# Performance work log

Hardware: AMD Instinct MI355X
Metric: run time of the kernel (lower is better)

Reference implementation:

```python
import jax, jax.numpy as jnp
import numpy as np

B, T, D, H = 4, 1024, 1024, 16
HD = D // H  # 64
EPS = 1e-5


def _layernorm(x, g, b):
    mu = jnp.mean(x, axis=-1, keepdims=True)
    var = jnp.mean(jnp.square(x - mu), axis=-1, keepdims=True)
    return (x - mu) * jax.lax.rsqrt(var + EPS) * g + b


def _apply_rope(x, cos, sin):
    # x: (B, H, T, HD); cos/sin: (T, HD//2)
    d = x.shape[-1] // 2
    x1, x2 = x[..., :d], x[..., d:]
    cos = cos[None, None]
    sin = sin[None, None]
    return jnp.concatenate([x1 * cos - x2 * sin, x1 * sin + x2 * cos], axis=-1)


def setup_inputs() -> dict:
    key = jax.random.key(0)
    ks = jax.random.split(key, 8)
    s = 0.02
    x = jax.random.normal(ks[0], (B, T, D), jnp.float32)
    # RoPE tables
    pos = jnp.arange(T, dtype=jnp.float32)
    inv_freq = 1.0 / (10000.0 ** (jnp.arange(HD // 2, dtype=jnp.float32) / (HD // 2)))
    ang = pos[:, None] * inv_freq[None, :]  # (T, HD//2)
    rope_cos, rope_sin = jnp.cos(ang), jnp.sin(ang)
    # causal mask: True = masked out (module does ~attn_mask before SDPA)
    attn_mask = jnp.triu(jnp.ones((T, T), dtype=bool), k=1)
    params = dict(
        ln1_g=jnp.ones((D,), jnp.float32), ln1_b=jnp.zeros((D,), jnp.float32),
        w_qkv=jax.random.normal(ks[1], (D, 3 * D), jnp.float32) * s,
        b_qkv=jnp.zeros((3 * D,), jnp.float32),
        w_out=jax.random.normal(ks[2], (D, D), jnp.float32) * s,
        b_out=jnp.zeros((D,), jnp.float32),
        ln2_g=jnp.ones((D,), jnp.float32), ln2_b=jnp.zeros((D,), jnp.float32),
        w1=jax.random.normal(ks[3], (D, 4 * D), jnp.float32) * s,
        b1=jnp.zeros((4 * D,), jnp.float32),
        w2=jax.random.normal(ks[4], (4 * D, D), jnp.float32) * s,
        b2=jnp.zeros((D,), jnp.float32),
    )
    return dict(x=x, attn_mask=attn_mask, rope_cos=rope_cos, rope_sin=rope_sin, **params)


def reference(x, attn_mask, rope_cos, rope_sin, ln1_g, ln1_b, w_qkv, b_qkv,
              w_out, b_out, ln2_g, ln2_b, w1, b1, w2, b2):
    b, t, d = x.shape
    h = _layernorm(x, ln1_g, ln1_b)
    qkv = (h @ w_qkv + b_qkv).reshape(b, t, 3, H, HD)
    q, k, v = jnp.transpose(qkv, (2, 0, 3, 1, 4))  # each (B, H, T, HD)
    q = _apply_rope(q, rope_cos, rope_sin)
    k = _apply_rope(k, rope_cos, rope_sin)
    scale = 1.0 / jnp.sqrt(jnp.asarray(HD, x.dtype))
    scores = jnp.einsum('bhqd,bhkd->bhqk', q, k) * scale
    allowed = ~attn_mask  # True = attend
    neg = jnp.finfo(scores.dtype).min
    scores = jnp.where(allowed[None, None], scores, neg)
    probs = jax.nn.softmax(scores, axis=-1)
    attn = jnp.einsum('bhqk,bhkd->bhqd', probs, v)
    attn = jnp.transpose(attn, (0, 2, 1, 3)).reshape(b, t, d)
    x = x + (attn @ w_out + b_out)
    h2 = _layernorm(x, ln2_g, ln2_b)
    mlp = jax.nn.gelu(h2 @ w1 + b1, approximate=False) @ w2 + b2
    return x + mlp
```

## Files before the change

### kernel.cpp

```cpp
#include <hip/hip_runtime.h>
#include <hip/hip_bf16.h>
#include <cstdint>


typedef __bf16 bf16x8_t __attribute__((ext_vector_type(8)));
typedef float  f32x4_t  __attribute__((ext_vector_type(4)));

#define MFMA16(a, b, c) __builtin_amdgcn_mfma_f32_16x16x32_bf16((a), (b), (c), 0, 0, 0)

static constexpr int Bb = 4, T = 1024, D = 1024, NH = 16, HD = 64;
static constexpr int ROWS = Bb * T;
static constexpr int QKVN = 3 * D;

__device__ __forceinline__ float bf2f(__hip_bfloat16 v) { return __bfloat162float(v); }
__device__ __forceinline__ ushort f2bfbits(float v) {
    __hip_bfloat16 h = __float2bfloat16(v);
    return *reinterpret_cast<ushort*>(&h);
}
__device__ __forceinline__ float loadf(const void* p, size_t i, int isb16) {
    return isb16 ? bf2f(((const __hip_bfloat16*)p)[i]) : ((const float*)p)[i];
}
__device__ __forceinline__ int dtype16(const void* gref) {
    return (((const unsigned*)gref)[0] & 0xFFFFu) != 0u;
}
__device__ __forceinline__ void gld_lds16(const __hip_bfloat16* g, __hip_bfloat16* l) {
    __builtin_amdgcn_global_load_lds(
        (const __attribute__((address_space(1))) void*)g,
        (__attribute__((address_space(3))) void*)l, 16, 0, 0);
}

__device__ __forceinline__ void trans_tile(const void* B, __hip_bfloat16* BT,
                                           int K, int N, int k0, int n0, int isb16) {
    __shared__ ushort t[64][68];
#pragma unroll
    for (int it = 0; it < 4; ++it) {
        int gi = threadIdx.x + it * 256;
        int r = gi >> 4, c4 = (gi & 15) * 4;
        if (isb16) {
            ushort4 v = *reinterpret_cast<const ushort4*>(
                (const __hip_bfloat16*)B + (size_t)(k0 + r) * N + n0 + c4);
            t[c4 + 0][r] = v.x; t[c4 + 1][r] = v.y;
            t[c4 + 2][r] = v.z; t[c4 + 3][r] = v.w;
        } else {
            float4 v = *reinterpret_cast<const float4*>(
                (const float*)B + (size_t)(k0 + r) * N + n0 + c4);
            t[c4 + 0][r] = f2bfbits(v.x); t[c4 + 1][r] = f2bfbits(v.y);
            t[c4 + 2][r] = f2bfbits(v.z); t[c4 + 3][r] = f2bfbits(v.w);
        }
    }
    __syncthreads();
#pragma unroll
    for (int it = 0; it < 4; ++it) {
        int gi = threadIdx.x + it * 256;
        int r = gi >> 4, c4 = (gi & 15) * 4;
        ushort4 v;
        v.x = t[r][c4]; v.y = t[r][c4 + 1]; v.z = t[r][c4 + 2]; v.w = t[r][c4 + 3];
        *reinterpret_cast<ushort4*>(
            reinterpret_cast<ushort*>(BT) + (size_t)(n0 + r) * K + k0 + c4) = v;
    }
}

__device__ __forceinline__ void ln_row(const void* x, const void* g, const void* bt,
                                       __hip_bfloat16* out, int row, int isb16) {
    const int tid = threadIdx.x;
    const int lane = tid & 63, w = tid >> 6;

    float v[4];
    if (isb16) {
        ushort4 raw = reinterpret_cast<const ushort4*>((const __hip_bfloat16*)x + (size_t)row * D)[tid];
        v[0] = __uint_as_float(((unsigned)raw.x) << 16);
        v[1] = __uint_as_float(((unsigned)raw.y) << 16);
        v[2] = __uint_as_float(((unsigned)raw.z) << 16);
        v[3] = __uint_as_float(((unsigned)raw.w) << 16);
    } else {
        float4 f = reinterpret_cast<const float4*>((const float*)x + (size_t)row * D)[tid];
        v[0] = f.x; v[1] = f.y; v[2] = f.z; v[3] = f.w;
    }

    float s1 = v[0] + v[1] + v[2] + v[3];
    float s2 = v[0] * v[0] + v[1] * v[1] + v[2] * v[2] + v[3] * v[3];
#pragma unroll
    for (int off = 32; off >= 1; off >>= 1) {
        s1 += __shfl_xor(s1, off, 64);
        s2 += __shfl_xor(s2, off, 64);
    }
    __shared__ float r1[4], r2[4];
    if (lane == 0) { r1[w] = s1; r2[w] = s2; }
    __syncthreads();
    float t1 = r1[0] + r1[1] + r1[2] + r1[3];
    float t2 = r2[0] + r2[1] + r2[2] + r2[3];
    float mu  = t1 * (1.0f / D);
    float var = t2 * (1.0f / D) - mu * mu;
    float rstd = rsqrtf(var + 1e-5f);

    const int c = tid * 4;
#pragma unroll
    for (int j = 0; j < 4; j++) {
        float gv = loadf(g, c + j, isb16), bv = loadf(bt, c + j, isb16);
        out[(size_t)row * D + c + j] = __float2bfloat16((v[j] - mu) * rstd * gv + bv);
    }
}

__global__ __launch_bounds__(256) void transpose_k(const void* __restrict__ B,
                                                   __hip_bfloat16* __restrict__ BT,
                                                   const void* __restrict__ gref,
                                                   int K, int N) {
    trans_tile(B, BT, K, N, blockIdx.y * 64, blockIdx.x * 64, dtype16(gref));
}

__global__ __launch_bounds__(256) void fusedpre_k(const void* w_qkv, const void* w_out,
                                                  const void* w1, const void* w2,
                                                  __hip_bfloat16* wqkvT, __hip_bfloat16* woutT,
                                                  __hip_bfloat16* w1T, __hip_bfloat16* w2T,
                                                  const void* __restrict__ x,
                                                  const void* __restrict__ ln_g,
                                                  const void* __restrict__ ln_b,
                                                  __hip_bfloat16* __restrict__ ln_out,
                                                  const void* __restrict__ gref) {
    const int isb16 = dtype16(gref);
    int bid = blockIdx.x;
    if (bid < 3072) {
        const void* src; __hip_bfloat16* dst; int K, N, l;
        if (bid < 768)       { src = w_qkv; dst = wqkvT; K = 1024; N = 3072; l = bid; }
        else if (bid < 1024) { src = w_out; dst = woutT; K = 1024; N = 1024; l = bid - 768; }
        else if (bid < 2048) { src = w1;    dst = w1T;   K = 1024; N = 4096; l = bid - 1024; }
        else                 { src = w2;    dst = w2T;   K = 4096; N = 1024; l = bid - 2048; }
        const int nb = N / 64;
        trans_tile(src, dst, K, N, (l / nb) * 64, (l % nb) * 64, isb16);
    } else {
        ln_row(x, ln_g, ln_b, ln_out, bid - 3072, isb16);
    }
}

__global__ __launch_bounds__(256) void ln_k(const void* __restrict__ x,
                                            const void* __restrict__ g,
                                            const void* __restrict__ bt,
                                            __hip_bfloat16* __restrict__ out,
                                            const void* __restrict__ gref) {
    ln_row(x, g, bt, out, blockIdx.x, dtype16(gref));
}

template <int MODE, bool SPLIT>
__global__ __launch_bounds__(512, 2) void gemm256_k(const __hip_bfloat16* __restrict__ A,
                                                    const __hip_bfloat16* __restrict__ BT,
                                                    const void* __restrict__ bias,
                                                    void* __restrict__ C,
                                                    const void* __restrict__ gref,
                                                    int M, int N, int Kstride, int klen) {
    extern __shared__ __hip_bfloat16 LDSb[];

    const int tid  = threadIdx.x;
    const int lane = tid & 63, w = tid >> 6;
    const int quad = lane >> 4, l15 = lane & 15;
    const int n0 = blockIdx.x * 256, m0 = blockIdx.y * 256;
    const int wmL = (w >> 2) * 128;
    const int wnL = (w & 3) * 64;
    const int kbase = SPLIT ? blockIdx.z * klen : 0;
    const int NT = klen >> 5;

    const int L0 = w * 1024 + lane * 16;
    const int L1 = L0 + 8192;
    const int r0 = L0 >> 6,  k0e = ((L0 & 63) ^ (((L0 >> 9) & 1) << 5)) >> 1;
    const int r1 = L1 >> 6,  k1e = ((L1 & 63) ^ (((L1 >> 9) & 1) << 5)) >> 1;
    const __hip_bfloat16* AgS0 = A  + (size_t)(m0 + r0) * Kstride + kbase + k0e;
    const __hip_bfloat16* AgS1 = A  + (size_t)(m0 + r1) * Kstride + kbase + k1e;
    const __hip_bfloat16* BgS0 = BT + (size_t)(n0 + r0) * Kstride + kbase + k0e;
    const __hip_bfloat16* BgS1 = BT + (size_t)(n0 + r1) * Kstride + kbase + k1e;
    const int ldst0 = w * 512, ldst1 = w * 512 + 4096;

    const int kofs = (quad * 8) ^ ((l15 & 8) << 1);

    f32x4_t acc[8][4] = {};

#pragma unroll
    for (int t = 0; t < 3; ++t) {
        __hip_bfloat16* sA = LDSb + t * 8192;
        __hip_bfloat16* sB = LDSb + 32768 + t * 8192;
        const int ko = t * 32;
        gld_lds16(AgS0 + ko, sA + ldst0);
        gld_lds16(AgS1 + ko, sA + ldst1);
        gld_lds16(BgS0 + ko, sB + ldst0);
        gld_lds16(BgS1 + ko, sB + ldst1);
    }
    asm volatile("s_waitcnt vmcnt(8)" ::: "memory");
    __builtin_amdgcn_s_barrier();
    __builtin_amdgcn_sched_barrier(0);

    for (int t = 0; t < NT; ++t) {
        if (t) {
            if (t + 2 < NT)      { asm volatile("s_waitcnt vmcnt(8)" ::: "memory"); }
            else if (t + 1 < NT) { asm volatile("s_waitcnt vmcnt(4)" ::: "memory"); }
            else                 { asm volatile("s_waitcnt vmcnt(0)" ::: "memory"); }
            __builtin_amdgcn_s_barrier();
            __builtin_amdgcn_sched_barrier(0);
        }
        if (t + 3 < NT) {
            const int sl = (t + 3) & 3;
            __hip_bfloat16* sA = LDSb + sl * 8192;
            __hip_bfloat16* sB = LDSb + 32768 + sl * 8192;
            const int ko = (t + 3) * 32;
            gld_lds16(AgS0 + ko, sA + ldst0);
            gld_lds16(AgS1 + ko, sA + ldst1);
            gld_lds16(BgS0 + ko, sB + ldst0);
            gld_lds16(BgS1 + ko, sB + ldst1);
        }

        const __hip_bfloat16* sA = LDSb + (t & 3) * 8192;
        const __hip_bfloat16* sB = LDSb + 32768 + (t & 3) * 8192;
        bf16x8_t a[8], b[4];
#pragma unroll
        for (int mf = 0; mf < 8; ++mf)
            a[mf] = *reinterpret_cast<const bf16x8_t*>(&sA[(wmL + mf * 16 + l15) * 32 + kofs]);
#pragma unroll
        for (int nf = 0; nf < 4; ++nf)
            b[nf] = *reinterpret_cast<const bf16x8_t*>(&sB[(wnL + nf * 16 + l15) * 32 + kofs]);
        __builtin_amdgcn_s_setprio(1);
#pragma unroll
        for (int mf = 0; mf < 8; ++mf)
#pragma unroll
            for (int nf = 0; nf < 4; ++nf)
                acc[mf][nf] = MFMA16(a[mf], b[nf], acc[mf][nf]);
        __builtin_amdgcn_s_setprio(0);
    }

    __syncthreads();

    __hip_bfloat16* Cb;
    if constexpr (SPLIT) {
        const int z = blockIdx.z;
        if (z == 0)      Cb = (__hip_bfloat16*)C;
        else if (z == 1) Cb = (__hip_bfloat16*)C + (size_t)M * N;
        else if (z == 2) Cb = (__hip_bfloat16*)const_cast<void*>(bias);
        else             Cb = (__hip_bfloat16*)const_cast<void*>(gref);
    } else {
        Cb = (__hip_bfloat16*)C;
    }
    const int isb16 = (MODE == 3) ? 0 : dtype16(gref);
    __hip_bfloat16* E = LDSb;
#pragma unroll
    for (int nf = 0; nf < 4; ++nf) {
        const int cc = wnL + nf * 16 + l15;
        const float bsv = (MODE == 3) ? 0.0f : loadf(bias, n0 + cc, isb16);
#pragma unroll
        for (int mf = 0; mf < 8; ++mf) {
            const int rbase = wmL + mf * 16 + quad * 4;
#pragma unroll
            for (int r = 0; r < 4; ++r) {
                const int rr = rbase + r;
                float v = acc[mf][nf][r] + bsv;
                if constexpr (MODE == 2)
                    v = 0.5f * v * (1.0f + erff(v * 0.70710678118654752f));
                E[rr * 256 + ((cc + (((rr >> 2) & 15) << 4)) & 255)] = __float2bfloat16(v);
            }
        }
    }
    __syncthreads();
#pragma unroll
    for (int it = 0; it < 16; ++it) {
        const int r = it * 16 + (tid >> 5), c = (tid & 31) * 8;
        const int cs = (c + (((r >> 2) & 15) << 4)) & 255;
        uint4 d = *reinterpret_cast<const uint4*>(&E[r * 256 + cs]);
        *reinterpret_cast<uint4*>(&Cb[(size_t)(m0 + r) * N + n0 + c]) = d;
    }
}

template <int MODE, bool SPLIT>
__global__ __launch_bounds__(256) void gemm_k(const __hip_bfloat16* __restrict__ A,
                                              const __hip_bfloat16* __restrict__ BT,
                                              const void* __restrict__ bias,
                                              void* __restrict__ C,
                                              const void* __restrict__ gref,
                                              int M, int N, int Kstride, int klen,
                                              const void* __restrict__ rc,
                                              const void* __restrict__ rs,
                                              __hip_bfloat16* __restrict__ vT) {
    __shared__ __hip_bfloat16 LB[16384];

    const int tid  = threadIdx.x;
    const int lane = tid & 63, w = tid >> 6;
    const int quad = lane >> 4, l15 = lane & 15;
    const int n0 = blockIdx.x * 128, m0 = blockIdx.y * 128;
    const int wm = (w >> 1) * 64, wn = (w & 1) * 64;
    const int kbase = SPLIT ? blockIdx.z * klen : 0;

    const int srow = lane >> 2, skk = (lane & 3) * 8;
    const __hip_bfloat16* Ag = A  + (size_t)(m0 + w * 16 + srow) * Kstride + kbase + skk;
    const __hip_bfloat16* Bg = BT + (size_t)(n0 + w * 16 + srow) * Kstride + kbase + skk;
    const int lwb = (w * 16) * 32;

    f32x4_t acc[4][4] = {};

    gld_lds16(Ag,                LB + lwb);
    gld_lds16(Ag + 64 * Kstride, LB + lwb + 64 * 32);
    gld_lds16(Bg,                LB + 8192 + lwb);
    gld_lds16(Bg + 64 * Kstride, LB + 8192 + lwb + 64 * 32);
    __syncthreads();

    int p = 0;
    for (int k0 = 0; k0 < klen; k0 += 32) {
        if (k0 + 32 < klen) {
            __hip_bfloat16* An = LB + (p ^ 1) * 4096;
            __hip_bfloat16* Bn = LB + 8192 + (p ^ 1) * 4096;
            gld_lds16(Ag + k0 + 32,                An + lwb);
            gld_lds16(Ag + k0 + 32 + 64 * Kstride, An + lwb + 64 * 32);
            gld_lds16(Bg + k0 + 32,                Bn + lwb);
            gld_lds16(Bg + k0 + 32 + 64 * Kstride, Bn + lwb + 64 * 32);
        }

        const __hip_bfloat16* Ac = LB + p * 4096;
        const __hip_bfloat16* Bc = LB + 8192 + p * 4096;
        bf16x8_t af[4], bfr[4];
#pragma unroll
        for (int t = 0; t < 4; t++) {
            af[t]  = *reinterpret_cast<const bf16x8_t*>(&Ac[(wm + t * 16 + l15) * 32 + quad * 8]);
            bfr[t] = *reinterpret_cast<const bf16x8_t*>(&Bc[(wn + t * 16 + l15) * 32 + quad * 8]);
        }
#pragma unroll
        for (int i = 0; i < 4; i++)
#pragma unroll
            for (int j = 0; j < 4; j++)
                acc[i][j] = MFMA16(af[i], bfr[j], acc[i][j]);

        __syncthreads();
        p ^= 1;
    }

    __hip_bfloat16* Cb;
    if constexpr (SPLIT) {
        const int z = blockIdx.z;
        if (z == 0)      Cb = (__hip_bfloat16*)C;
        else if (z == 1) Cb = (__hip_bfloat16*)C + (size_t)M * N;
        else if (z == 2) Cb = (__hip_bfloat16*)const_cast<void*>(bias);
        else             Cb = (__hip_bfloat16*)const_cast<void*>(gref);
    } else {
        Cb = (__hip_bfloat16*)C;
    }
    const int isb16 = (MODE == 3) ? 0 : dtype16(gref);
    __hip_bfloat16* E = LB;

    if constexpr (MODE == 1) {
        const int sec = n0 >> 10;
#pragma unroll
        for (int j = 0; j < 2; j++) {
            const int cc0 = wn + j * 16 + l15;
            const int cc2 = cc0 + 32;
            const float bs0 = loadf(bias, n0 + cc0, isb16);
            const float bs2 = loadf(bias, n0 + cc2, isb16);
            const int d = j * 16 + l15;
#pragma unroll
            for (int i = 0; i < 4; i++) {
                const int rbase = wm + i * 16 + quad * 4;
#pragma unroll
                for (int r = 0; r < 4; r++) {
                    const int rr = rbase + r;
                    float v0 = acc[i][j][r] + bs0;
                    float v2 = acc[i][j + 2][r] + bs2;
                    if (sec < 2) {
                        const int t = (m0 + rr) & (T - 1);
                        const float cv = loadf(rc, (size_t)t * 32 + d, isb16);
                        const float sv = loadf(rs, (size_t)t * 32 + d, isb16);
                        float o0 = v0 * cv - v2 * sv;
                        float o2 = v0 * sv + v2 * cv;
                        if (sec == 0) { o0 *= 0.125f; o2 *= 0.125f; }
                        v0 = o0; v2 = o2;
                    }
                    E[rr * 128 + ((cc0 + (((rr >> 2) & 7) << 4)) & 127)] = __float2bfloat16(v0);
                    E[rr * 128 + ((cc2 + (((rr >> 2) & 7) << 4)) & 127)] = __float2bfloat16(v2);
                }
            }
        }
    } else {
#pragma unroll
        for (int j = 0; j < 4; j++) {
            const int cc = wn + j * 16 + l15;
            const float bsv = (MODE == 3) ? 0.0f : loadf(bias, n0 + cc, isb16);
#pragma unroll
            for (int i = 0; i < 4; i++) {
                const int rbase = wm + i * 16 + quad * 4;
#pragma unroll
                for (int r = 0; r < 4; r++) {
                    const int rr = rbase + r;
                    float v = acc[i][j][r] + bsv;
                    if constexpr (MODE == 2)
                        v = 0.5f * v * (1.0f + erff(v * 0.70710678118654752f));
                    E[rr * 128 + ((cc + (((rr >> 2) & 7) << 4)) & 127)] = __float2bfloat16(v);
                }
            }
        }
    }
    __syncthreads();
#pragma unroll
    for (int it = 0; it < 8; it++) {
        const int r = it * 16 + (tid >> 4), c = (tid & 15) * 8;
        const int cs = (c + (((r >> 2) & 7) << 4)) & 127;
        uint4 d = *reinterpret_cast<const uint4*>(&E[r * 128 + cs]);
        *reinterpret_cast<uint4*>(&Cb[(size_t)(m0 + r) * N + n0 + c]) = d;
    }

    if constexpr (MODE == 1) {
        if (n0 >= 2 * D) {
            const int bq  = m0 >> 10;
            const int t0  = m0 & (T - 1);
            const int n0v = n0 - 2 * D;
#pragma unroll
            for (int it = 0; it < 8; ++it) {
                const int idx = tid + it * 256;
                const int f   = idx >> 4;
                const int tg  = (idx & 15) * 8;
                alignas(16) ushort pk[8];
#pragma unroll
                for (int kk = 0; kk < 8; ++kk) {
                    const int tt = tg + kk;
                    pk[kk] = reinterpret_cast<const ushort*>(E)[
                        tt * 128 + ((f + (((tt >> 2) & 7) << 4)) & 127)];
                }
                *reinterpret_cast<uint4*>(
                    &vT[((size_t)(bq * 1024 + n0v + f)) * T + t0 + tg]) =
                    *reinterpret_cast<const uint4*>(pk);
            }
        }
    }
}

__global__ __launch_bounds__(256) void reduce4_k(const __hip_bfloat16* __restrict__ p0,
                                                 const __hip_bfloat16* __restrict__ p1,
                                                 const __hip_bfloat16* __restrict__ p2,
                                                 const __hip_bfloat16* __restrict__ p3,
                                                 const void* __restrict__ bias,
                                                 const void* __restrict__ res,
                                                 void* __restrict__ out,
                                                 const void* __restrict__ gref) {
    const int isb16 = dtype16(gref);
    const size_t i = ((size_t)blockIdx.x * 256 + threadIdx.x) * 4;
    ushort4 a = *reinterpret_cast<const ushort4*>(p0 + i);
    ushort4 b = *reinterpret_cast<const ushort4*>(p1 + i);
    ushort4 c = *reinterpret_cast<const ushort4*>(p2 + i);
    ushort4 d = *reinterpret_cast<const ushort4*>(p3 + i);
    const int col = (int)(i & (D - 1));
    float v[4];
    v[0] = __uint_as_float((unsigned)a.x << 16) + __uint_as_float((unsigned)b.x << 16)
         + __uint_as_float((unsigned)c.x << 16) + __uint_as_float((unsigned)d.x << 16);
    v[1] = __uint_as_float((unsigned)a.y << 16) + __uint_as_float((unsigned)b.y << 16)
         + __uint_as_float((unsigned)c.y << 16) + __uint_as_float((unsigned)d.y << 16);
    v[2] = __uint_as_float((unsigned)a.z << 16) + __uint_as_float((unsigned)b.z << 16)
         + __uint_as_float((unsigned)c.z << 16) + __uint_as_float((unsigned)d.z << 16);
    v[3] = __uint_as_float((unsigned)a.w << 16) + __uint_as_float((unsigned)b.w << 16)
         + __uint_as_float((unsigned)c.w << 16) + __uint_as_float((unsigned)d.w << 16);
#pragma unroll
    for (int j = 0; j < 4; j++)
        v[j] += loadf(bias, col + j, isb16) + loadf(res, i + j, isb16);
    if (isb16) {
        ushort4 o;
        o.x = f2bfbits(v[0]); o.y = f2bfbits(v[1]); o.z = f2bfbits(v[2]); o.w = f2bfbits(v[3]);
        *reinterpret_cast<ushort4*>((__hip_bfloat16*)out + i) = o;
    } else {
        float4 o = {v[0], v[1], v[2], v[3]};
        *reinterpret_cast<float4*>((float*)out + i) = o;
    }
}

__global__ __launch_bounds__(256) void gemm64_k(const __hip_bfloat16* __restrict__ A,
                                                const __hip_bfloat16* __restrict__ BT,
                                                const void* __restrict__ bias,
                                                const void* __restrict__ res,
                                                void* __restrict__ C,
                                                const void* __restrict__ gref,
                                                int M, int N, int K, int crow0) {
    __shared__ __hip_bfloat16 LB64[12288];

    const int tid  = threadIdx.x;
    const int lane = tid & 63, w = tid >> 6;
    const int quad = lane >> 4, l15 = lane & 15;
    const int n0 = blockIdx.x * 64, m0 = blockIdx.y * 128;
    const int wm = (w >> 1) * 64, wn = (w & 1) * 32;

    const int srow = lane >> 2, skk = (lane & 3) * 8;
    const __hip_bfloat16* Ag = A  + (size_t)(m0 + w * 16 + srow) * K + skk;
    const __hip_bfloat16* Bg = BT + (size_t)(n0 + w * 16 + srow) * K + skk;
    const int lwb = (w * 16) * 32;

    f32x4_t acc[4][2] = {};

    gld_lds16(Ag,          LB64 + lwb);
    gld_lds16(Ag + 64 * K, LB64 + lwb + 64 * 32);
    gld_lds16(Bg,          LB64 + 8192 + lwb);
    __syncthreads();

    int p = 0;
    for (int k0 = 0; k0 < K; k0 += 32) {
        if (k0 + 32 < K) {
            __hip_bfloat16* An = LB64 + (p ^ 1) * 4096;
            __hip_bfloat16* Bn = LB64 + 8192 + (p ^ 1) * 2048;
            gld_lds16(Ag + k0 + 32,          An + lwb);
            gld_lds16(Ag + k0 + 32 + 64 * K, An + lwb + 64 * 32);
            gld_lds16(Bg + k0 + 32,          Bn + lwb);
        }

        const __hip_bfloat16* Ac = LB64 + p * 4096;
        const __hip_bfloat16* Bc = LB64 + 8192 + p * 2048;
        bf16x8_t af[4], bfr[2];
#pragma unroll
        for (int t = 0; t < 4; t++)
            af[t]  = *reinterpret_cast<const bf16x8_t*>(&Ac[(wm + t * 16 + l15) * 32 + quad * 8]);
#pragma unroll
        for (int t = 0; t < 2; t++)
            bfr[t] = *reinterpret_cast<const bf16x8_t*>(&Bc[(wn + t * 16 + l15) * 32 + quad * 8]);
#pragma unroll
        for (int i = 0; i < 4; i++)
#pragma unroll
            for (int j = 0; j < 2; j++)
                acc[i][j] = MFMA16(af[i], bfr[j], acc[i][j]);

        __syncthreads();
        p ^= 1;
    }

    const int isb16 = dtype16(gref);
    __hip_bfloat16* E = LB64;
#pragma unroll
    for (int j = 0; j < 2; j++) {
        const int cc = wn + j * 16 + l15;
        const float bsv = loadf(bias, n0 + cc, isb16);
#pragma unroll
        for (int i = 0; i < 4; i++) {
            const int rbase = wm + i * 16 + quad * 4;
#pragma unroll
            for (int r = 0; r < 4; r++) {
                const int rr = rbase + r;
                E[rr * 64 + ((cc + (((rr >> 2) & 7) << 4)) & 63)] =
                    __float2bfloat16(acc[i][j][r] + bsv);
            }
        }
    }
    __syncthreads();
#pragma unroll
    for (int it = 0; it < 4; it++) {
        const int r = it * 32 + (tid >> 3), c = (tid & 7) * 8;
        const int cs = (c + (((r >> 2) & 7) << 4)) & 63;
        const size_t gr = (size_t)(crow0 + m0 + r);
        alignas(16) ushort pk[8];
        *reinterpret_cast<uint4*>(pk) = *reinterpret_cast<const uint4*>(&E[r * 64 + cs]);
        if (isb16) {
            const ushort4 rv0 = *reinterpret_cast<const ushort4*>(
                (const __hip_bfloat16*)res + gr * N + n0 + c);
            const ushort4 rv1 = *reinterpret_cast<const ushort4*>(
                (const __hip_bfloat16*)res + gr * N + n0 + c + 4);
            const ushort rvs[8] = {rv0.x, rv0.y, rv0.z, rv0.w, rv1.x, rv1.y, rv1.z, rv1.w};
            alignas(16) ushort o[8];
#pragma unroll
            for (int k = 0; k < 8; k++)
                o[k] = f2bfbits(__uint_as_float((unsigned)pk[k] << 16) +
                                __uint_as_float((unsigned)rvs[k] << 16));
            *reinterpret_cast<uint4*>((__hip_bfloat16*)C + gr * N + n0 + c) =
                *reinterpret_cast<const uint4*>(o);
        } else {
            const float4 r0 = *reinterpret_cast<const float4*>(
                (const float*)res + gr * N + n0 + c);
            const float4 r1 = *reinterpret_cast<const float4*>(
                (const float*)res + gr * N + n0 + c + 4);
            const float rf[8] = {r0.x, r0.y, r0.z, r0.w, r1.x, r1.y, r1.z, r1.w};
            float ov[8];
#pragma unroll
            for (int k = 0; k < 8; k++)
                ov[k] = __uint_as_float((unsigned)pk[k] << 16) + rf[k];
            float4 s0 = {ov[0], ov[1], ov[2], ov[3]};
            float4 s1 = {ov[4], ov[5], ov[6], ov[7]};
            *reinterpret_cast<float4*>((float*)C + gr * N + n0 + c)     = s0;
            *reinterpret_cast<float4*>((float*)C + gr * N + n0 + c + 4) = s1;
        }
    }
}

__global__ __launch_bounds__(256) void ropevt_k(__hip_bfloat16* __restrict__ qkv,
                                                const void* __restrict__ rc,
                                                const void* __restrict__ rs,
                                                __hip_bfloat16* __restrict__ vT,
                                                const void* __restrict__ gref) {
    const int bid = blockIdx.x;
    if (bid < 8192) {
        const int isb16 = dtype16(gref);
        const int id = bid * 256 + threadIdx.x;
        const int d  = id & 31;
        const int h  = (id >> 5) & 15;
        const int t  = (id >> 9) & 1023;
        const int b  = id >> 19;
        const float c = loadf(rc, t * 32 + d, isb16);
        const float s = loadf(rs, t * 32 + d, isb16);
        __hip_bfloat16* base = qkv + ((size_t)(b * T + t)) * QKVN + h * HD + d;
        float x1 = bf2f(base[0]), x2 = bf2f(base[32]);
        base[0]  = __float2bfloat16((x1 * c - x2 * s) * 0.125f);
        base[32] = __float2bfloat16((x1 * s + x2 * c) * 0.125f);
        float y1 = bf2f(base[D]), y2 = bf2f(base[D + 32]);
        base[D]      = __float2bfloat16(y1 * c - y2 * s);
        base[D + 32] = __float2bfloat16(y1 * s + y2 * c);
    } else {
        __shared__ ushort t[64][65];
        const int l = bid - 8192;
        const int t0 = (l & 15) * 64, bh = l >> 4;
        const int b = bh >> 4, h = bh & 15;
        const __hip_bfloat16* src = qkv + ((size_t)b * T) * QKVN + 2 * D + h * HD;
#pragma unroll
        for (int it = 0; it < 16; ++it) {
            int idx = threadIdx.x + it * 256;
            int r = idx >> 6, d = idx & 63;
            t[d][r] = *reinterpret_cast<const ushort*>(src + (size_t)(t0 + r) * QKVN + d);
        }
        __syncthreads();
#pragma unroll
        for (int it = 0; it < 16; ++it) {
            int idx = threadIdx.x + it * 256;
            int r = idx >> 6, c = idx & 63;
            reinterpret_cast<ushort*>(vT)[((size_t)bh * 64 + r) * T + t0 + c] = t[r][c];
        }
    }
}

__global__ __launch_bounds__(256) void flash_k(const __hip_bfloat16* __restrict__ qkv,
                                               const __hip_bfloat16* __restrict__ vT,
                                               __hip_bfloat16* __restrict__ out) {
    __shared__ __hip_bfloat16 Qs[2][64 * 32];
    __shared__ __hip_bfloat16 Ks[2][2][64 * 32];
    __shared__ __hip_bfloat16 Vs[2][2][64 * 32];
    __shared__ __hip_bfloat16 Ps[4][2][16 * 32];

    const int tid = threadIdx.x;
    const int bid = blockIdx.x;
    const int qt = 15 - (bid >> 6);
    const int bh = bid & 63;
    const int b = bh >> 4, h = bh & 15;
    const int q0 = qt * 64;
    const int lane = tid & 63, w = tid >> 6, quad = lane >> 4, l15 = lane & 15;
    const int srow = lane >> 2, skk = (lane & 3) * 8;

    const __hip_bfloat16* qg = qkv + ((size_t)(b * T) + q0 + w * 16 + srow) * QKVN + h * HD + skk;
    const __hip_bfloat16* kg = qkv + ((size_t)(b * T) + w * 16 + srow) * QKVN + D + h * HD + skk;
    const __hip_bfloat16* vg = vT + ((size_t)bh * 64 + w * 16 + srow) * T + skk;

    gld_lds16(qg,      &Qs[0][(w * 16) * 32]);
    gld_lds16(qg + 32, &Qs[1][(w * 16) * 32]);
    gld_lds16(kg,      &Ks[0][0][(w * 16) * 32]);
    gld_lds16(kg + 32, &Ks[0][1][(w * 16) * 32]);
    gld_lds16(vg,      &Vs[0][0][(w * 16) * 32]);
    gld_lds16(vg + 32, &Vs[0][1][(w * 16) * 32]);
    __syncthreads();

    const bf16x8_t aq0 = *reinterpret_cast<const bf16x8_t*>(&Qs[0][(w * 16 + l15) * 32 + quad * 8]);
    const bf16x8_t aq1 = *reinterpret_cast<const bf16x8_t*>(&Qs[1][(w * 16 + l15) * 32 + quad * 8]);

    float m_run[4], l_run[4];
    f32x4_t o[4] = {};
#pragma unroll
    for (int i = 0; i < 4; i++) { m_run[i] = -1e30f; l_run[i] = 0.0f; }

    int p = 0;
    for (int kt = 0; kt <= qt; kt++) {
        if (kt < qt) {
            const size_t ko = (size_t)(kt + 1) * 64;
            gld_lds16(kg + ko * QKVN,      &Ks[p ^ 1][0][(w * 16) * 32]);
            gld_lds16(kg + ko * QKVN + 32, &Ks[p ^ 1][1][(w * 16) * 32]);
            gld_lds16(vg + ko,             &Vs[p ^ 1][0][(w * 16) * 32]);
            gld_lds16(vg + ko + 32,        &Vs[p ^ 1][1][(w * 16) * 32]);
        }

        f32x4_t s[4];
#pragma unroll
        for (int c = 0; c < 4; c++) {
            f32x4_t z = {};
            bf16x8_t k0f = *reinterpret_cast<const bf16x8_t*>(&Ks[p][0][(c * 16 + l15) * 32 + quad * 8]);
            bf16x8_t k1f = *reinterpret_cast<const bf16x8_t*>(&Ks[p][1][(c * 16 + l15) * 32 + quad * 8]);
            z = MFMA16(aq0, k0f, z);
            z = MFMA16(aq1, k1f, z);
            s[c] = z;
        }

        if (kt == qt) {
#pragma unroll
            for (int c = 0; c < 4; c++)
#pragma unroll
                for (int i = 0; i < 4; i++) {
                    int rr = w * 16 + quad * 4 + i;
                    int cc = c * 16 + l15;
                    if (cc > rr) s[c][i] = -1e30f;
                }
        }

        float mnew[4], alpha[4];
#pragma unroll
        for (int i = 0; i < 4; i++) {
            float mx = fmaxf(fmaxf(s[0][i], s[1][i]), fmaxf(s[2][i], s[3][i]));
#pragma unroll
            for (int off = 1; off < 16; off <<= 1) mx = fmaxf(mx, __shfl_xor(mx, off, 64));
            mnew[i] = fmaxf(m_run[i], mx);
            alpha[i] = __expf(m_run[i] - mnew[i]);
            m_run[i] = mnew[i];
        }
#pragma unroll
        for (int c = 0; c < 4; c++)
#pragma unroll
            for (int i = 0; i < 4; i++) s[c][i] = __expf(s[c][i] - mnew[i]);
#pragma unroll
        for (int i = 0; i < 4; i++) {
            float sm = s[0][i] + s[1][i] + s[2][i] + s[3][i];
#pragma unroll
            for (int off = 1; off < 16; off <<= 1) sm += __shfl_xor(sm, off, 64);
            l_run[i] = l_run[i] * alpha[i] + sm;
#pragma unroll
            for (int od = 0; od < 4; od++) o[od][i] *= alpha[i];
        }

#pragma unroll
        for (int c = 0; c < 4; c++)
#pragma unroll
            for (int i = 0; i < 4; i++)
                Ps[w][c >> 1][(quad * 4 + i) * 32 + (c & 1) * 16 + l15] =
                    __float2bfloat16(s[c][i]);

        bf16x8_t ap0 = *reinterpret_cast<const bf16x8_t*>(&Ps[w][0][l15 * 32 + quad * 8]);
        bf16x8_t ap1 = *reinterpret_cast<const bf16x8_t*>(&Ps[w][1][l15 * 32 + quad * 8]);
#pragma unroll
        for (int od = 0; od < 4; od++) {
            bf16x8_t v0f = *reinterpret_cast<const bf16x8_t*>(&Vs[p][0][(od * 16 + l15) * 32 + quad * 8]);
            bf16x8_t v1f = *reinterpret_cast<const bf16x8_t*>(&Vs[p][1][(od * 16 + l15) * 32 + quad * 8]);
            o[od] = MFMA16(ap0, v0f, o[od]);
            o[od] = MFMA16(ap1, v1f, o[od]);
        }

        __syncthreads();
        p ^= 1;
    }

#pragma unroll
    for (int od = 0; od < 4; od++)
#pragma unroll
        for (int i = 0; i < 4; i++) {
            int row = q0 + w * 16 + quad * 4 + i;
            int col = h * HD + od * 16 + l15;
            float v = o[od][i] / l_run[i];
            out[((size_t)b * T + row) * D + col] = __float2bfloat16(v);
        }
}

extern "C" void kernel_launch(void* const* d_in, const int* in_sizes, int n_in,
                              void* d_out, int out_size, void* d_ws, size_t ws_size,
                              hipStream_t stream) {
    const int o = (in_sizes[1] == T * (HD / 2)) ? 1 : 2;
    const void* x     = d_in[0];
    const void* rc    = d_in[o + 0];
    const void* rs    = d_in[o + 1];
    const void* ln1g  = d_in[o + 2];
    const void* ln1b  = d_in[o + 3];
    const void* w_qkv = d_in[o + 4];
    const void* b_qkv = d_in[o + 5];
    const void* w_out = d_in[o + 6];
    const void* b_out = d_in[o + 7];
    const void* ln2g  = d_in[o + 8];
    const void* ln2b  = d_in[o + 9];
    const void* w1    = d_in[o + 10];
    const void* b1    = d_in[o + 11];
    const void* w2    = d_in[o + 12];
    const void* b2    = d_in[o + 13];

    char* ws = (char*)d_ws;
    const size_t MB = 1024 * 1024;

    static bool attr_done = false;
    if (!attr_done) {
        hipFuncSetAttribute(reinterpret_cast<const void*>(&gemm256_k<2, false>),
                            hipFuncAttributeMaxDynamicSharedMemorySize, 131072);
        hipFuncSetAttribute(reinterpret_cast<const void*>(&gemm256_k<3, true>),
                            hipFuncAttributeMaxDynamicSharedMemorySize, 131072);
        attr_done = true;
    }

    if (ws_size >= 72 * MB + 256) {
        __hip_bfloat16* bufA  = (__hip_bfloat16*)(ws + 256);
        __hip_bfloat16* qkvb  = (__hip_bfloat16*)(ws + 8 * MB + 256);
        __hip_bfloat16* vTb   = (__hip_bfloat16*)(ws + 32 * MB + 256);
        __hip_bfloat16* mid   = qkvb;
        __hip_bfloat16* wqkvT = (__hip_bfloat16*)(ws + 40 * MB + 256);
        __hip_bfloat16* woutT = (__hip_bfloat16*)(ws + 46 * MB + 256);
        __hip_bfloat16* w1T   = (__hip_bfloat16*)(ws + 48 * MB + 256);
        __hip_bfloat16* w2T   = (__hip_bfloat16*)(ws + 56 * MB + 256);
        __hip_bfloat16* part0 = (__hip_bfloat16*)(ws + 40 * MB + 256);
        __hip_bfloat16* part2 = (__hip_bfloat16*)(ws + 64 * MB + 256);
        __hip_bfloat16* part1 = (__hip_bfloat16*)(ws + 48 * MB + 256);
        __hip_bfloat16* part3 = bufA;

        fusedpre_k<<<3072 + ROWS, 256, 0, stream>>>(w_qkv, w_out, w1, w2,
                                                    wqkvT, woutT, w1T, w2T,
                                                    x, ln1g, ln1b, bufA, ln1g);
        gemm_k<1, false><<<dim3(QKVN / 128, ROWS / 128), 256, 0, stream>>>(
            bufA, wqkvT, b_qkv, qkvb, ln1g, ROWS, QKVN, D, D, rc, rs, vTb);
        flash_k<<<16 * Bb * NH, 256, 0, stream>>>(qkvb, vTb, bufA);
        gemm64_k<<<dim3(D / 64, ROWS / 128), 256, 0, stream>>>(bufA, woutT, b_out, x,
                                                               d_out, ln1g, ROWS, D, D, 0);
        ln_k<<<ROWS, 256, 0, stream>>>(d_out, ln2g, ln2b, bufA, ln1g);
        gemm256_k<2, false><<<dim3(4 * D / 256, ROWS / 256), 512, 131072, stream>>>(
            bufA, w1T, b1, mid, ln1g, ROWS, 4 * D, D, D);
        gemm256_k<3, true><<<dim3(D / 256, ROWS / 256, 4), 512, 131072, stream>>>(
            mid, w2T, part2, part0, part3, ROWS, D, 4 * D, D);
        reduce4_k<<<(ROWS * D) / (256 * 4), 256, 0, stream>>>(part0, part1, part2, part3,
                                                              b2, d_out, d_out, ln1g);
    } else {
        __hip_bfloat16* bufA  = (__hip_bfloat16*)(ws + 256);
        __hip_bfloat16* qkvb  = (__hip_bfloat16*)(ws + 8 * MB + 256);
        __hip_bfloat16* wqkvT = (__hip_bfloat16*)(ws + 32 * MB + 256);
        __hip_bfloat16* vTb   = (__hip_bfloat16*)(ws + 32 * MB + 256);
        __hip_bfloat16* woutT = (__hip_bfloat16*)(ws + 8 * MB + 256);
        __hip_bfloat16* w1T   = (__hip_bfloat16*)(ws + 8 * MB + 256);
        __hip_bfloat16* w2T   = (__hip_bfloat16*)(ws + 16 * MB + 256);
        __hip_bfloat16* mid   = (__hip_bfloat16*)(ws + 24 * MB + 256);

        transpose_k<<<dim3(QKVN / 64, D / 64), 256, 0, stream>>>(w_qkv, wqkvT, ln1g, D, QKVN);
        ln_k<<<ROWS, 256, 0, stream>>>(x, ln1g, ln1b, bufA, ln1g);
        gemm_k<0, false><<<dim3(QKVN / 128, ROWS / 128), 256, 0, stream>>>(
            bufA, wqkvT, b_qkv, qkvb, ln1g, ROWS, QKVN, D, D, nullptr, nullptr, nullptr);
        ropevt_k<<<8192 + 1024, 256, 0, stream>>>(qkvb, rc, rs, vTb, ln1g);
        flash_k<<<16 * Bb * NH, 256, 0, stream>>>(qkvb, vTb, bufA);
        transpose_k<<<dim3(D / 64, D / 64), 256, 0, stream>>>(w_out, woutT, ln1g, D, D);
        gemm64_k<<<dim3(D / 64, ROWS / 128), 256, 0, stream>>>(bufA, woutT, b_out, x,
                                                               d_out, ln1g, ROWS, D, D, 0);
        ln_k<<<ROWS, 256, 0, stream>>>(d_out, ln2g, ln2b, bufA, ln1g);
        transpose_k<<<dim3(4 * D / 64, D / 64), 256, 0, stream>>>(w1, w1T, ln1g, D, 4 * D);
        transpose_k<<<dim3(D / 64, 4 * D / 64), 256, 0, stream>>>(w2, w2T, ln1g, 4 * D, D);
        for (int c = 0; c < 2; c++) {
            const int ro = c * 2048;
            gemm_k<2, false><<<dim3(4 * D / 128, 2048 / 128), 256, 0, stream>>>(
                bufA + (size_t)ro * D, w1T, b1, mid, ln1g, 2048, 4 * D, D, D,
                nullptr, nullptr, nullptr);
            gemm64_k<<<dim3(D / 64, 2048 / 128), 256, 0, stream>>>(mid, w2T, b2, d_out,
                                                                   d_out, ln1g, 2048, D, 4 * D, ro);
        }
    }
}
```

Before: 359.3 us.

## Move weight transposes into flash-attention tail blocks and vectorize LN/reduce stores

Removes the out-proj and MLP weight transposes from the pre-pass kernel and runs them as extra blocks appended to the flash attention launch, sharing one LDS buffer. The aim is to overlap transpose bandwidth work with the imbalanced causal attention tail and to shorten the serial pre-kernel ahead of the QKV GEMM. Layernorm output and the split-K reduce bias/residual loads are also vectorized. Flash LDS usage is unified into one array, and the transpose blocks may compete with attention blocks for CUs.

Measured after the change: 354.2 us. No clear change (-1.4%).

```diff
diff --git a/kernel.cpp b/kernel.cpp
--- a/kernel.cpp
+++ b/kernel.cpp
@@ -29,9 +29,9 @@
         (__attribute__((address_space(3))) void*)l, 16, 0, 0);
 }
 
-__device__ __forceinline__ void trans_tile(const void* B, __hip_bfloat16* BT,
-                                           int K, int N, int k0, int n0, int isb16) {
-    __shared__ ushort t[64][68];
+__device__ __forceinline__ void trans_tile_core(ushort* sc, const void* B,
+                                                __hip_bfloat16* BT,
+                                                int K, int N, int k0, int n0, int isb16) {
 #pragma unroll
     for (int it = 0; it < 4; ++it) {
         int gi = threadIdx.x + it * 256;
@@ -39,13 +39,13 @@
         if (isb16) {
             ushort4 v = *reinterpret_cast<const ushort4*>(
                 (const __hip_bfloat16*)B + (size_t)(k0 + r) * N + n0 + c4);
-            t[c4 + 0][r] = v.x; t[c4 + 1][r] = v.y;
-            t[c4 + 2][r] = v.z; t[c4 + 3][r] = v.w;
+            sc[(c4 + 0) * 68 + r] = v.x; sc[(c4 + 1) * 68 + r] = v.y;
+            sc[(c4 + 2) * 68 + r] = v.z; sc[(c4 + 3) * 68 + r] = v.w;
         } else {
             float4 v = *reinterpret_cast<const float4*>(
                 (const float*)B + (size_t)(k0 + r) * N + n0 + c4);
-            t[c4 + 0][r] = f2bfbits(v.x); t[c4 + 1][r] = f2bfbits(v.y);
-            t[c4 + 2][r] = f2bfbits(v.z); t[c4 + 3][r] = f2bfbits(v.w);
+            sc[(c4 + 0) * 68 + r] = f2bfbits(v.x); sc[(c4 + 1) * 68 + r] = f2bfbits(v.y);
+            sc[(c4 + 2) * 68 + r] = f2bfbits(v.z); sc[(c4 + 3) * 68 + r] = f2bfbits(v.w);
         }
     }
     __syncthreads();
@@ -53,11 +53,16 @@
     for (int it = 0; it < 4; ++it) {
         int gi = threadIdx.x + it * 256;
         int r = gi >> 4, c4 = (gi & 15) * 4;
-        ushort4 v;
-        v.x = t[r][c4]; v.y = t[r][c4 + 1]; v.z = t[r][c4 + 2]; v.w = t[r][c4 + 3];
+        ushort4 v = *reinterpret_cast<const ushort4*>(&sc[r * 68 + c4]);
         *reinterpret_cast<ushort4*>(
             reinterpret_cast<ushort*>(BT) + (size_t)(n0 + r) * K + k0 + c4) = v;
     }
+}
+
+__device__ __forceinline__ void trans_tile(const void* B, __hip_bfloat16* BT,
+                                           int K, int N, int k0, int n0, int isb16) {
+    __shared__ ushort t[64 * 68];
+    trans_tile_core(t, B, BT, K, N, k0, n0, isb16);
 }
 
 __device__ __forceinline__ void ln_row(const void* x, const void* g, const void* bt,
@@ -94,11 +99,19 @@
     float rstd = rsqrtf(var + 1e-5f);
 
     const int c = tid * 4;
-#pragma unroll
-    for (int j = 0; j < 4; j++) {
-        float gv = loadf(g, c + j, isb16), bv = loadf(bt, c + j, isb16);
-        out[(size_t)row * D + c + j] = __float2bfloat16((v[j] - mu) * rstd * gv + bv);
-    }
+    ushort4 o;
+    {
+        float gv, bv;
+        gv = loadf(g, c + 0, isb16); bv = loadf(bt, c + 0, isb16);
+        o.x = f2bfbits((v[0] - mu) * rstd * gv + bv);
+        gv = loadf(g, c + 1, isb16); bv = loadf(bt, c + 1, isb16);
+        o.y = f2bfbits((v[1] - mu) * rstd * gv + bv);
+        gv = loadf(g, c + 2, isb16); bv = loadf(bt, c + 2, isb16);
+        o.z = f2bfbits((v[2] - mu) * rstd * gv + bv);
+        gv = loadf(g, c + 3, isb16); bv = loadf(bt, c + 3, isb16);
+        o.w = f2bfbits((v[3] - mu) * rstd * gv + bv);
+    }
+    *reinterpret_cast<ushort4*>(out + (size_t)row * D + c) = o;
 }
 
 __global__ __launch_bounds__(256) void transpose_k(const void* __restrict__ B,
@@ -108,10 +121,8 @@
     trans_tile(B, BT, K, N, blockIdx.y * 64, blockIdx.x * 64, dtype16(gref));
 }
 
-__global__ __launch_bounds__(256) void fusedpre_k(const void* w_qkv, const void* w_out,
-                                                  const void* w1, const void* w2,
-                                                  __hip_bfloat16* wqkvT, __hip_bfloat16* woutT,
-                                                  __hip_bfloat16* w1T, __hip_bfloat16* w2T,
+__global__ __launch_bounds__(256) void fusedpre_k(const void* w_qkv,
+                                                  __hip_bfloat16* wqkvT,
                                                   const void* __restrict__ x,
                                                   const void* __restrict__ ln_g,
                                                   const void* __restrict__ ln_b,
@@ -119,16 +130,11 @@
                                                   const void* __restrict__ gref) {
     const int isb16 = dtype16(gref);
     int bid = blockIdx.x;
-    if (bid < 3072) {
-        const void* src; __hip_bfloat16* dst; int K, N, l;
-        if (bid < 768)       { src = w_qkv; dst = wqkvT; K = 1024; N = 3072; l = bid; }
-        else if (bid < 1024) { src = w_out; dst = woutT; K = 1024; N = 1024; l = bid - 768; }
-        else if (bid < 2048) { src = w1;    dst = w1T;   K = 1024; N = 4096; l = bid - 1024; }
-        else                 { src = w2;    dst = w2T;   K = 4096; N = 1024; l = bid - 2048; }
-        const int nb = N / 64;
-        trans_tile(src, dst, K, N, (l / nb) * 64, (l % nb) * 64, isb16);
+    if (bid < 768) {
+        const int nb = QKVN / 64;
+        trans_tile(w_qkv, wqkvT, D, QKVN, (bid / nb) * 64, (bid % nb) * 64, isb16);
     } else {
-        ln_row(x, ln_g, ln_b, ln_out, bid - 3072, isb16);
+        ln_row(x, ln_g, ln_b, ln_out, bid - 768, isb16);
     }
 }
 
@@ -446,9 +452,22 @@
          + __uint_as_float((unsigned)c.z << 16) + __uint_as_float((unsigned)d.z << 16);
     v[3] = __uint_as_float((unsigned)a.w << 16) + __uint_as_float((unsigned)b.w << 16)
          + __uint_as_float((unsigned)c.w << 16) + __uint_as_float((unsigned)d.w << 16);
-#pragma unroll
-    for (int j = 0; j < 4; j++)
-        v[j] += loadf(bias, col + j, isb16) + loadf(res, i + j, isb16);
+    float bv[4], rv[4];
+    if (isb16) {
+        ushort4 bb = *reinterpret_cast<const ushort4*>((const __hip_bfloat16*)bias + col);
+        ushort4 rr = *reinterpret_cast<const ushort4*>((const __hip_bfloat16*)res + i);
+        bv[0] = __uint_as_float((unsigned)bb.x << 16); bv[1] = __uint_as_float((unsigned)bb.y << 16);
+        bv[2] = __uint_as_float((unsigned)bb.z << 16); bv[3] = __uint_as_float((unsigned)bb.w << 16);
+        rv[0] = __uint_as_float((unsigned)rr.x << 16); rv[1] = __uint_as_float((unsigned)rr.y << 16);
+        rv[2] = __uint_as_float((unsigned)rr.z << 16); rv[3] = __uint_as_float((unsigned)rr.w << 16);
+    } else {
+        float4 bb = *reinterpret_cast<const float4*>((const float*)bias + col);
+        float4 rr = *reinterpret_cast<const float4*>((const float*)res + i);
+        bv[0] = bb.x; bv[1] = bb.y; bv[2] = bb.z; bv[3] = bb.w;
+        rv[0] = rr.x; rv[1] = rr.y; rv[2] = rr.z; rv[3] = rr.w;
+    }
+#pragma unroll
+    for (int j = 0; j < 4; j++) v[j] += bv[j] + rv[j];
     if (isb16) {
         ushort4 o;
         o.x = f2bfbits(v[0]); o.y = f2bfbits(v[1]); o.z = f2bfbits(v[2]); o.w = f2bfbits(v[3]);
@@ -617,14 +636,35 @@
 
 __global__ __launch_bounds__(256) void flash_k(const __hip_bfloat16* __restrict__ qkv,
                                                const __hip_bfloat16* __restrict__ vT,
-                                               __hip_bfloat16* __restrict__ out) {
-    __shared__ __hip_bfloat16 Qs[2][64 * 32];
-    __shared__ __hip_bfloat16 Ks[2][2][64 * 32];
-    __shared__ __hip_bfloat16 Vs[2][2][64 * 32];
-    __shared__ __hip_bfloat16 Ps[4][2][16 * 32];
-
+                                               __hip_bfloat16* __restrict__ out,
+                                               const void* __restrict__ w_out,
+                                               const void* __restrict__ w1,
+                                               const void* __restrict__ w2,
+                                               __hip_bfloat16* __restrict__ woutT,
+                                               __hip_bfloat16* __restrict__ w1T,
+                                               __hip_bfloat16* __restrict__ w2T,
+                                               const void* __restrict__ gref) {
+    __shared__ __hip_bfloat16 FL[24576];
     const int tid = threadIdx.x;
     const int bid = blockIdx.x;
+
+    if (bid >= 1024) {
+        const int l = bid - 1024;
+        const void* src; __hip_bfloat16* dst; int K, N, ll;
+        if (l < 256)       { src = w_out; dst = woutT; K = 1024; N = 1024; ll = l; }
+        else if (l < 1280) { src = w1;    dst = w1T;   K = 1024; N = 4096; ll = l - 256; }
+        else               { src = w2;    dst = w2T;   K = 4096; N = 1024; ll = l - 1280; }
+        const int nb = N / 64;
+        trans_tile_core(reinterpret_cast<ushort*>(FL), src, dst, K, N,
+                        (ll / nb) * 64, (ll % nb) * 64, dtype16(gref));
+        return;
+    }
+
+    __hip_bfloat16* Qsb = FL;
+    __hip_bfloat16* Ksb = FL + 4096;
+    __hip_bfloat16* Vsb = FL + 12288;
+    __hip_bfloat16* Psb = FL + 20480;
+
     const int qt = 15 - (bid >> 6);
     const int bh = bid & 63;
     const int b = bh >> 4, h = bh & 15;
@@ -636,16 +676,16 @@
     const __hip_bfloat16* kg = qkv + ((size_t)(b * T) + w * 16 + srow) * QKVN + D + h * HD + skk;
     const __hip_bfloat16* vg = vT + ((size_t)bh * 64 + w * 16 + srow) * T + skk;
 
-    gld_lds16(qg,      &Qs[0][(w * 16) * 32]);
-    gld_lds16(qg + 32, &Qs[1][(w * 16) * 32]);
-    gld_lds16(kg,      &Ks[0][0][(w * 16) * 32]);
-    gld_lds16(kg + 32, &Ks[0][1][(w * 16) * 32]);
-    gld_lds16(vg,      &Vs[0][0][(w * 16) * 32]);
-    gld_lds16(vg + 32, &Vs[0][1][(w * 16) * 32]);
+    gld_lds16(qg,      Qsb + (w * 16) * 32);
+    gld_lds16(qg + 32, Qsb + 2048 + (w * 16) * 32);
+    gld_lds16(kg,      Ksb + (w * 16) * 32);
+    gld_lds16(kg + 32, Ksb + 2048 + (w * 16) * 32);
+    gld_lds16(vg,      Vsb + (w * 16) * 32);
+    gld_lds16(vg + 32, Vsb + 2048 + (w * 16) * 32);
     __syncthreads();
 
-    const bf16x8_t aq0 = *reinterpret_cast<const bf16x8_t*>(&Qs[0][(w * 16 + l15) * 32 + quad * 8]);
-    const bf16x8_t aq1 = *reinterpret_cast<const bf16x8_t*>(&Qs[1][(w * 16 + l15) * 32 + quad * 8]);
+    const bf16x8_t aq0 = *reinterpret_cast<const bf16x8_t*>(&Qsb[(w * 16 + l15) * 32 + quad * 8]);
+    const bf16x8_t aq1 = *reinterpret_cast<const bf16x8_t*>(&Qsb[2048 + (w * 16 + l15) * 32 + quad * 8]);
 
     float m_run[4], l_run[4];
     f32x4_t o[4] = {};
@@ -656,18 +696,23 @@
     for (int kt = 0; kt <= qt; kt++) {
         if (kt < qt) {
             const size_t ko = (size_t)(kt + 1) * 64;
-            gld_lds16(kg + ko * QKVN,      &Ks[p ^ 1][0][(w * 16) * 32]);
-            gld_lds16(kg + ko * QKVN + 32, &Ks[p ^ 1][1][(w * 16) * 32]);
-            gld_lds16(vg + ko,             &Vs[p ^ 1][0][(w * 16) * 32]);
-            gld_lds16(vg + ko + 32,        &Vs[p ^ 1][1][(w * 16) * 32]);
-        }
+            __hip_bfloat16* Kn = Ksb + (p ^ 1) * 4096;
+            __hip_bfloat16* Vn = Vsb + (p ^ 1) * 4096;
+            gld_lds16(kg + ko * QKVN,      Kn + (w * 16) * 32);
+            gld_lds16(kg + ko * QKVN + 32, Kn + 2048 + (w * 16) * 32);
+            gld_lds16(vg + ko,             Vn + (w * 16) * 32);
+            gld_lds16(vg + ko + 32,        Vn + 2048 + (w * 16) * 32);
+        }
+
+        const __hip_bfloat16* Kc = Ksb + p * 4096;
+        const __hip_bfloat16* Vc = Vsb + p * 4096;
 
         f32x4_t s[4];
 #pragma unroll
         for (int c = 0; c < 4; c++) {
             f32x4_t z = {};
-            bf16x8_t k0f = *reinterpret_cast<const bf16x8_t*>(&Ks[p][0][(c * 16 + l15) * 32 + quad * 8]);
-            bf16x8_t k1f = *reinterpret_cast<const bf16x8_t*>(&Ks[p][1][(c * 16 + l15) * 32 + quad * 8]);
+            bf16x8_t k0f = *reinterpret_cast<const bf16x8_t*>(&Kc[(c * 16 + l15) * 32 + quad * 8]);
+            bf16x8_t k1f = *reinterpret_cast<const bf16x8_t*>(&Kc[2048 + (c * 16 + l15) * 32 + quad * 8]);
             z = MFMA16(aq0, k0f, z);
             z = MFMA16(aq1, k1f, z);
             s[c] = z;
@@ -708,19 +753,20 @@
             for (int od = 0; od < 4; od++) o[od][i] *= alpha[i];
         }
 
+        __hip_bfloat16* Pw = Psb + w * 1024;
 #pragma unroll
         for (int c = 0; c < 4; c++)
 #pragma unroll
             for (int i = 0; i < 4; i++)
-                Ps[w][c >> 1][(quad * 4 + i) * 32 + (c & 1) * 16 + l15] =
+                Pw[(c >> 1) * 512 + (quad * 4 + i) * 32 + (c & 1) * 16 + l15] =
                     __float2bfloat16(s[c][i]);
 
-        bf16x8_t ap0 = *reinterpret_cast<const bf16x8_t*>(&Ps[w][0][l15 * 32 + quad * 8]);
-        bf16x8_t ap1 = *reinterpret_cast<const bf16x8_t*>(&Ps[w][1][l15 * 32 + quad * 8]);
+        bf16x8_t ap0 = *reinterpret_cast<const bf16x8_t*>(&Pw[l15 * 32 + quad * 8]);
+        bf16x8_t ap1 = *reinterpret_cast<const bf16x8_t*>(&Pw[512 + l15 * 32 + quad * 8]);
 #pragma unroll
         for (int od = 0; od < 4; od++) {
-            bf16x8_t v0f = *reinterpret_cast<const bf16x8_t*>(&Vs[p][0][(od * 16 + l15) * 32 + quad * 8]);
-            bf16x8_t v1f = *reinterpret_cast<const bf16x8_t*>(&Vs[p][1][(od * 16 + l15) * 32 + quad * 8]);
+            bf16x8_t v0f = *reinterpret_cast<const bf16x8_t*>(&Vc[(od * 16 + l15) * 32 + quad * 8]);
+            bf16x8_t v1f = *reinterpret_cast<const bf16x8_t*>(&Vc[2048 + (od * 16 + l15) * 32 + quad * 8]);
             o[od] = MFMA16(ap0, v0f, o[od]);
             o[od] = MFMA16(ap1, v1f, o[od]);
         }
@@ -786,12 +832,12 @@
         __hip_bfloat16* part1 = (__hip_bfloat16*)(ws + 48 * MB + 256);
         __hip_bfloat16* part3 = bufA;
 
-        fusedpre_k<<<3072 + ROWS, 256, 0, stream>>>(w_qkv, w_out, w1, w2,
-                                                    wqkvT, woutT, w1T, w2T,
-                                                    x, ln1g, ln1b, bufA, ln1g);
+        fusedpre_k<<<768 + ROWS, 256, 0, stream>>>(w_qkv, wqkvT,
+                                                   x, ln1g, ln1b, bufA, ln1g);
         gemm_k<1, false><<<dim3(QKVN / 128, ROWS / 128), 256, 0, stream>>>(
             bufA, wqkvT, b_qkv, qkvb, ln1g, ROWS, QKVN, D, D, rc, rs, vTb);
-        flash_k<<<16 * Bb * NH, 256, 0, stream>>>(qkvb, vTb, bufA);
+        flash_k<<<1024 + 2304, 256, 0, stream>>>(qkvb, vTb, bufA,
+                                                 w_out, w1, w2, woutT, w1T, w2T, ln1g);
         gemm64_k<<<dim3(D / 64, ROWS / 128), 256, 0, stream>>>(bufA, woutT, b_out, x,
                                                                d_out, ln1g, ROWS, D, D, 0);
         ln_k<<<ROWS, 256, 0, stream>>>(d_out, ln2g, ln2b, bufA, ln1g);
@@ -816,7 +862,9 @@
         gemm_k<0, false><<<dim3(QKVN / 128, ROWS / 128), 256, 0, stream>>>(
             bufA, wqkvT, b_qkv, qkvb, ln1g, ROWS, QKVN, D, D, nullptr, nullptr, nullptr);
         ropevt_k<<<8192 + 1024, 256, 0, stream>>>(qkvb, rc, rs, vTb, ln1g);
-        flash_k<<<16 * Bb * NH, 256, 0, stream>>>(qkvb, vTb, bufA);
+        flash_k<<<1024, 256, 0, stream>>>(qkvb, vTb, bufA,
+                                          nullptr, nullptr, nullptr,
+                                          nullptr, nullptr, nullptr, ln1g);
         transpose_k<<<dim3(D / 64, D / 64), 256, 0, stream>>>(w_out, woutT, ln1g, D, D);
         gemm64_k<<<dim3(D / 64, ROWS / 128), 256, 0, stream>>>(bufA, woutT, b_out, x,
                                                                d_out, ln1g, ROWS, D, D, 0);
```
